# Kernel optimization log

Measured on AMD Instinct MI355X. Metric: run time of the kernel, lower is better.

The kernel has to match this reference:

```python
import jax, jax.numpy as jnp
import numpy as np

HEADS = 4
DIM_QK = 128
DIM_V = 128
FMAP = 32  # H = W = 32, L = 1024
DIM = 512
B = 16


def rel_to_abs(x):
    # x: [B, Nh, L, 2L-1] -> [B, Nh, L, L]
    b, nh, L, _ = x.shape
    x = jnp.pad(x, ((0, 0), (0, 0), (0, 0), (0, 1)))          # [B, Nh, L, 2L]
    flat = x.reshape(b, nh, L * 2 * L)
    flat = jnp.pad(flat, ((0, 0), (0, 0), (0, L - 1)))
    final = flat.reshape(b, nh, L + 1, 2 * L - 1)
    return final[:, :, :L, L - 1:]


def relative_logits_1d(q, rel_k):
    # q: [B, Nh, H, W, d], rel_k: [2W-1, d] -> [B, Nh, H, H, W, W]
    b, nh, h, w, _ = q.shape
    rl = jnp.einsum('bnhwd,md->bnhwm', q, rel_k)
    rl = rl.reshape(b, nh * h, w, 2 * w - 1)
    rl = rel_to_abs(rl)                                        # [B, Nh*H, W, W]
    rl = rl.reshape(b, nh, h, w, w)
    rl = jnp.broadcast_to(rl[:, :, :, None], (b, nh, h, h, w, w))
    return rl


def rel_pos_logits(q, rel_height, rel_width):
    # q: [B, Nh, L, d] with L = FMAP*FMAP -> [B, Nh, L, L]
    b, nh, L, d = q.shape
    h = w = FMAP
    q5 = q.reshape(b, nh, h, w, d)
    # width logits: 'b n x i y j -> b n (x y) (i j)'
    rw = relative_logits_1d(q5, rel_width)
    rw = rw.transpose(0, 1, 2, 4, 3, 5).reshape(b, nh, h * w, h * w)
    # height logits: transpose spatial, then 'b n x i y j -> b n (y x) (j i)'
    rh = relative_logits_1d(q5.transpose(0, 1, 3, 2, 4), rel_height)
    rh = rh.transpose(0, 1, 4, 2, 5, 3).reshape(b, nh, h * w, h * w)
    return rw + rh


def setup_inputs() -> dict:
    key = jax.random.key(0)
    k1, k2, k3, k4, k5 = jax.random.split(key, 5)
    scale = DIM_QK ** -0.5
    return {
        'featuremap': jax.random.normal(k1, (B, DIM, FMAP, FMAP), jnp.float32),
        'w_qk': jax.random.normal(k2, (2 * HEADS * DIM_QK, DIM), jnp.float32) * (DIM ** -0.5),
        'w_v': jax.random.normal(k3, (HEADS * DIM_V, DIM), jnp.float32) * (DIM ** -0.5),
        'rel_height': jax.random.normal(k4, (2 * FMAP - 1, DIM_QK), jnp.float32) * scale,
        'rel_width': jax.random.normal(k5, (2 * FMAP - 1, DIM_QK), jnp.float32) * scale,
    }


def reference(featuremap, w_qk, w_v, rel_height, rel_width):
    b, c, h, w = featuremap.shape
    L = h * w
    # 1x1 convs (no bias) == channel matmuls
    qk = jnp.einsum('bchw,oc->bohw', featuremap, w_qk)
    q, k = jnp.split(qk, 2, axis=1)
    v = jnp.einsum('bchw,oc->bohw', featuremap, w_v)

    def to_heads(x, d):
        # 'B (h d) H W -> B h (H W) d'
        return x.reshape(b, HEADS, d, L).transpose(0, 1, 3, 2)

    q = to_heads(q, DIM_QK) * (DIM_QK ** -0.5)
    k = to_heads(k, DIM_QK)
    v = to_heads(v, DIM_V)

    logits = jnp.einsum('bhxd,bhyd->bhxy', q, k)
    logits = logits + rel_pos_logits(q, rel_height, rel_width)
    weights = jax.nn.softmax(logits, axis=-1)
    attn = jnp.einsum('bhxy,bhyd->bhxd', weights, v)
    # 'B h (H W) d -> B (h d) H W'
    out = attn.transpose(0, 1, 3, 2).reshape(b, HEADS * DIM_V, h, w)
    return out
```

## Files before the change

### kernel.cpp

```cpp
#include <hip/hip_runtime.h>
#include <hip/hip_bf16.h>
#include <math.h>

typedef __bf16 bf16x8 __attribute__((ext_vector_type(8)));
typedef float f32x4 __attribute__((ext_vector_type(4)));

#define QSCALE_L2E (0.08838834764831845f * 1.4426950408889634f)

static __device__ __forceinline__ unsigned short bits_bf16(float v) {
  __hip_bfloat16 h = __float2bfloat16(v);
  return *reinterpret_cast<unsigned short*>(&h);
}

static __device__ __forceinline__ void gload16(const void* g, void* l) {
  __builtin_amdgcn_global_load_lds(
      (const __attribute__((address_space(1))) void*)g,
      (__attribute__((address_space(3))) void*)l, 16, 0, 0);
}

__global__ __launch_bounds__(256) void k_convw(const float* __restrict__ wqk,
                                               const float* __restrict__ wv,
                                               const float* __restrict__ relw,
                                               const float* __restrict__ relh,
                                               __hip_bfloat16* __restrict__ wall,
                                               __hip_bfloat16* __restrict__ relsb) {
  int i = blockIdx.x * 256 + threadIdx.x;
  if (i < 1536 * 512) {
    float v = (i < 1024 * 512) ? wqk[i] : wv[i - 1024 * 512];
    wall[i] = __float2bfloat16(v);
  } else {
    int j = i - 1536 * 512;
    int t = j >> 13, m = (j >> 7) & 63, d = j & 127;
    float v = (m < 63) ? (t ? relh[m * 128 + d] : relw[m * 128 + d]) : 0.f;
    relsb[j] = __float2bfloat16(v);
  }
}

__global__ __launch_bounds__(256) void k_tfm(const float* __restrict__ fm,
                                             __hip_bfloat16* __restrict__ fmt) {
  __shared__ float t[64][65];
  int lt = blockIdx.x, ct = blockIdx.y, b = blockIdx.z;
  int tid = threadIdx.x;
  const float* src = fm + ((size_t)b * 512 + ct * 64) * 1024 + lt * 64;
#pragma unroll
  for (int i = 0; i < 16; ++i) {
    int idx = i * 256 + tid;
    int r = idx >> 6, cl = idx & 63;
    t[r][cl] = src[(size_t)r * 1024 + cl];
  }
  __syncthreads();
  __hip_bfloat16* dst = fmt + ((size_t)b * 1024 + lt * 64) * 512 + ct * 64;
#pragma unroll
  for (int i = 0; i < 16; ++i) {
    int idx = i * 256 + tid;
    int r = idx >> 6, cc = idx & 63;
    dst[(size_t)r * 512 + cc] = __float2bfloat16(t[cc][r]);
  }
}

__global__ __launch_bounds__(256) void k_gemm(const __hip_bfloat16* __restrict__ fmt,
                                              const __hip_bfloat16* __restrict__ wall,
                                              __hip_bfloat16* __restrict__ Qb,
                                              __hip_bfloat16* __restrict__ Kb,
                                              __hip_bfloat16* __restrict__ Vt) {
  __shared__ char smem[32768];
  char* As = smem;
  char* Bs = smem + 16384;
  int bm = blockIdx.x, bn = blockIdx.y, b = blockIdx.z;
  int tid = threadIdx.x;
  int lane = tid & 63, wave = tid >> 6;
  int wr = wave >> 1, wc = wave & 1;
  int g = lane >> 4, ln = lane & 15;
  const char* Ag = (const char*)(fmt + ((size_t)b * 1024 + bm * 128) * 512);
  const char* Bg = (const char*)(wall + (size_t)bn * 128 * 512);

  int j3 = lane >> 3, j7 = lane & 7;
  int segsrc = ((j7 ^ j3) << 4);

  f32x4 acc[4][4] = {};
  for (int kb = 0; kb < 8; ++kb) {
#pragma unroll
    for (int i = 0; i < 4; ++i) {
      int R = (wave * 4 + i) * 8;
      size_t go = (size_t)(R + j3) * 1024 + (size_t)kb * 128 + segsrc;
      gload16(Ag + go, As + R * 128);
      gload16(Bg + go, Bs + R * 128);
    }
    __syncthreads();
#pragma unroll
    for (int ks = 0; ks < 2; ++ks) {
      int kcol = ks * 64 + (g << 4);
      bf16x8 af[4], bfr[4];
#pragma unroll
      for (int m = 0; m < 4; ++m) {
        int row = wr * 64 + m * 16 + ln;
        af[m] = *(const bf16x8*)(As + row * 128 + (kcol ^ ((ln & 7) << 4)));
      }
#pragma unroll
      for (int n = 0; n < 4; ++n) {
        int row = wc * 64 + n * 16 + ln;
        bfr[n] = *(const bf16x8*)(Bs + row * 128 + (kcol ^ ((ln & 7) << 4)));
      }
#pragma unroll
      for (int m = 0; m < 4; ++m)
#pragma unroll
        for (int n = 0; n < 4; ++n)
          acc[m][n] = __builtin_amdgcn_mfma_f32_16x16x32_bf16(af[m], bfr[n], acc[m][n], 0, 0, 0);
    }
    __syncthreads();
  }

  int otype = bn >> 2;
  int head = bn & 3;
  if (otype != 2) {
    float sc = (otype == 0) ? QSCALE_L2E : 1.0f;
#pragma unroll
    for (int m = 0; m < 4; ++m)
#pragma unroll
      for (int n = 0; n < 4; ++n) {
        int d = wc * 64 + n * 16 + ln;
#pragma unroll
        for (int r = 0; r < 4; ++r) {
          int l = wr * 64 + m * 16 + g * 4 + r;
          *(__hip_bfloat16*)(smem + l * 256 + ((d * 2) ^ ((l & 7) << 4))) =
              __float2bfloat16(acc[m][n][r] * sc);
        }
      }
    __syncthreads();
    __hip_bfloat16* dstb =
        (otype == 0 ? Qb : Kb) + (((size_t)(b * 4 + head) * 1024) + bm * 128) * 128;
#pragma unroll
    for (int i = 0; i < 8; ++i) {
      int idx = i * 256 + tid;
      int row = idx >> 4, c16 = idx & 15;
      uint4 v = *(const uint4*)(smem + row * 256 + ((c16 * 16) ^ ((row & 7) << 4)));
      *(uint4*)(dstb + (size_t)row * 128 + c16 * 8) = v;
    }
  } else {
#pragma unroll
    for (int m = 0; m < 4; ++m)
#pragma unroll
      for (int n = 0; n < 4; ++n) {
        int d = wc * 64 + n * 16 + ln;
        int lbase = wr * 64 + m * 16 + g * 4;
        ushort4 pk;
        pk.x = bits_bf16(acc[m][n][0]);
        pk.y = bits_bf16(acc[m][n][1]);
        pk.z = bits_bf16(acc[m][n][2]);
        pk.w = bits_bf16(acc[m][n][3]);
        *(ushort4*)(smem + d * 256 + ((lbase * 2) ^ ((d & 7) << 4))) = pk;
      }
    __syncthreads();
    __hip_bfloat16* dstb = Vt + ((size_t)(b * 4 + head) * 128) * 1024 + bm * 128;
#pragma unroll
    for (int i = 0; i < 8; ++i) {
      int idx = i * 256 + tid;
      int row = idx >> 4, c16 = idx & 15;
      uint4 v = *(const uint4*)(smem + row * 256 + ((c16 * 16) ^ ((row & 7) << 4)));
      *(uint4*)(dstb + (size_t)row * 1024 + c16 * 8) = v;
    }
  }
}

__global__ __launch_bounds__(256) void k_bias(const __hip_bfloat16* __restrict__ Qb,
                                              const __hip_bfloat16* __restrict__ relsb,
                                              float* __restrict__ QRW,
                                              float* __restrict__ QRH) {
  __shared__ char sh[32768];
  int bx = blockIdx.x, bh = blockIdx.y;
  int tid = threadIdx.x, lane = tid & 63, wave = tid >> 6;
  int g = lane >> 4, ln = lane & 15;
#pragma unroll
  for (int i = 0; i < 8; ++i) {
    int chunk = i * 256 + tid;
    int row = chunk >> 4, c16 = chunk & 15;
    *(uint4*)(sh + row * 256 + ((c16 * 16) ^ ((row & 7) << 4))) =
        *(const uint4*)(relsb + (size_t)row * 128 + c16 * 8);
  }
  __syncthreads();
  size_t bhL = (size_t)bh * 1024;
  int l0 = bx * 128 + wave * 32;
  const __hip_bfloat16* Qg = Qb + (bhL + l0) * 128;
  bf16x8 a[2][4];
#pragma unroll
  for (int lf = 0; lf < 2; ++lf)
#pragma unroll
    for (int ks = 0; ks < 4; ++ks)
      a[lf][ks] = *(const bf16x8*)(Qg + (size_t)(lf * 16 + ln) * 128 + ks * 32 + g * 8);
#pragma unroll
  for (int t = 0; t < 2; ++t) {
    float* dst = (t == 0 ? QRW : QRH) + (bhL + l0) * 64;
#pragma unroll
    for (int n = 0; n < 4; ++n) {
      f32x4 acc2[2] = {};
#pragma unroll
      for (int ks = 0; ks < 4; ++ks) {
        int mrow = n * 16 + ln;
        bf16x8 bf = *(const bf16x8*)(sh + t * 16384 + mrow * 256 +
                                     ((ks * 64 + g * 16) ^ ((mrow & 7) << 4)));
#pragma unroll
        for (int lf = 0; lf < 2; ++lf)
          acc2[lf] = __builtin_amdgcn_mfma_f32_16x16x32_bf16(a[lf][ks], bf, acc2[lf], 0, 0, 0);
      }
#pragma unroll
      for (int lf = 0; lf < 2; ++lf)
#pragma unroll
        for (int r = 0; r < 4; ++r)
          dst[(size_t)(lf * 16 + g * 4 + r) * 64 + n * 16 + ln] = acc2[lf][r];
    }
  }
}

__global__ __launch_bounds__(256) void k_attn(const __hip_bfloat16* __restrict__ Qb,
                                              const __hip_bfloat16* __restrict__ Kb,
                                              const __hip_bfloat16* __restrict__ Vt,
                                              const float* __restrict__ QRW,
                                              const float* __restrict__ QRH,
                                              float* __restrict__ out) {
  extern __shared__ char smem[];
  float* qrw_s = (float*)smem;
  float* qrh_s = (float*)(smem + 17408);
  char* kv = smem + 34816;
  char* vtl = smem + 51200;
  char* pt = smem + 67584;

  int qt = blockIdx.x, bh = blockIdx.y;
  int b = bh >> 2, h = bh & 3;
  int tid = threadIdx.x, lane = tid & 63, wave = tid >> 6;
  int g = lane >> 4, ln = lane & 15;
  int q0 = qt * 64;
  size_t bhL = (size_t)bh * 1024;

  const char* Qg = (const char*)(Qb + (bhL + q0) * 128);
#pragma unroll
  for (int i = 0; i < 4; ++i) {
    int R = (wave * 4 + i) * 4;
    int seg = ((lane & 15) ^ (((i & 1) * 4) + (lane >> 4))) << 4;
    gload16(Qg + (size_t)(R + (lane >> 4)) * 256 + seg, kv + R * 256);
  }
#pragma unroll
  for (int i = 0; i < 4; ++i) {
    int chunk = i * 256 + tid;
    int row = chunk >> 4, c16 = chunk & 15;
    *(uint4*)(qrw_s + row * 68 + c16 * 4) =
        *(const uint4*)(QRW + (bhL + q0 + row) * 64 + c16 * 4);
    *(uint4*)(qrh_s + row * 68 + c16 * 4) =
        *(const uint4*)(QRH + (bhL + q0 + row) * 64 + c16 * 4);
  }
  __syncthreads();

  bf16x8 qa[4];
  int qloc = wave * 16 + ln;
#pragma unroll
  for (int ks = 0; ks < 4; ++ks)
    qa[ks] = *(const bf16x8*)(kv + qloc * 256 + ((ks * 64 + (g << 4)) ^ ((qloc & 7) << 4)));

  int qg2 = q0 + qloc;
  int cx = qg2 & 31, rx = qg2 >> 5;
  float wb[2][4];
#pragma unroll
  for (int half = 0; half < 2; ++half)
#pragma unroll
    for (int r = 0; r < 4; ++r)
      wb[half][r] = qrw_s[qloc * 68 + (half * 16 + g * 4 + r - cx + 31)];
  const float* hptr = qrh_s + qloc * 68 + (31 - rx);

  f32x4 acc_o[8] = {};
  float mrow = -1e30f, lrow = 0.f;
  char* pw = pt + wave * 2048;
  const char* Kg0 = (const char*)(Kb + bhL * 128);
  const char* Vg0 = (const char*)(Vt + (size_t)bh * 128 * 1024);
  int j3 = lane >> 3, j7 = lane & 7;
  int segv = ((j7 ^ j3) << 4);

  for (int kt = 0; kt < 16; ++kt) {
    __syncthreads();
    const char* Kg = Kg0 + (size_t)kt * 64 * 256;
#pragma unroll
    for (int i = 0; i < 4; ++i) {
      int R = (wave * 4 + i) * 4;
      int seg = ((lane & 15) ^ (((i & 1) * 4) + (lane >> 4))) << 4;
      gload16(Kg + (size_t)(R + (lane >> 4)) * 256 + seg, kv + R * 256);
    }
    const char* Vg = Vg0 + (size_t)kt * 128;
#pragma unroll
    for (int i = 0; i < 4; ++i) {
      int R = (wave * 4 + i) * 8;
      gload16(Vg + (size_t)(R + j3) * 2048 + segv, vtl + R * 128);
    }
    __syncthreads();

    f32x4 s[4] = {};
#pragma unroll
    for (int ks = 0; ks < 4; ++ks) {
      int kcol = ks * 64 + (g << 4);
#pragma unroll
      for (int n = 0; n < 4; ++n) {
        int krow = n * 16 + ln;
        bf16x8 kf = *(const bf16x8*)(kv + krow * 256 + (kcol ^ ((krow & 7) << 4)));
        s[n] = __builtin_amdgcn_mfma_f32_16x16x32_bf16(kf, qa[ks], s[n], 0, 0, 0);
      }
    }
    float hb0 = hptr[kt * 2], hb1 = hptr[kt * 2 + 1];
#pragma unroll
    for (int n = 0; n < 4; ++n) {
      float hb = (n >> 1) ? hb1 : hb0;
#pragma unroll
      for (int r = 0; r < 4; ++r) s[n][r] += wb[n & 1][r] + hb;
    }
    float mt = s[0][0];
#pragma unroll
    for (int n = 0; n < 4; ++n)
#pragma unroll
      for (int r = 0; r < 4; ++r) mt = fmaxf(mt, s[n][r]);
    mt = fmaxf(mt, __shfl_xor(mt, 16, 64));
    mt = fmaxf(mt, __shfl_xor(mt, 32, 64));
    float mn = fmaxf(mrow, mt);
    float alpha = exp2f(mrow - mn);
    mrow = mn;
    float rs = 0.f;
#pragma unroll
    for (int n = 0; n < 4; ++n)
#pragma unroll
      for (int r = 0; r < 4; ++r) {
        s[n][r] = exp2f(s[n][r] - mrow);
        rs += s[n][r];
      }
    rs += __shfl_xor(rs, 16, 64);
    rs += __shfl_xor(rs, 32, 64);
    lrow = lrow * alpha + rs;
#pragma unroll
    for (int mf = 0; mf < 8; ++mf) acc_o[mf] *= alpha;
#pragma unroll
    for (int n = 0; n < 4; ++n) {
      ushort4 pk;
      pk.x = bits_bf16(s[n][0]);
      pk.y = bits_bf16(s[n][1]);
      pk.z = bits_bf16(s[n][2]);
      pk.w = bits_bf16(s[n][3]);
      *(ushort4*)(pw + ln * 128 + ((n * 32 + g * 8) ^ ((ln & 7) << 4))) = pk;
    }
#pragma unroll
    for (int ks2 = 0; ks2 < 2; ++ks2) {
      int kcb = ks2 * 64 + (g << 4);
      bf16x8 pb = *(const bf16x8*)(pw + ln * 128 + (kcb ^ ((ln & 7) << 4)));
#pragma unroll
      for (int mf = 0; mf < 8; ++mf) {
        int vrow = mf * 16 + ln;
        bf16x8 av = *(const bf16x8*)(vtl + vrow * 128 + (kcb ^ ((vrow & 7) << 4)));
        acc_o[mf] = __builtin_amdgcn_mfma_f32_16x16x32_bf16(av, pb, acc_o[mf], 0, 0, 0);
      }
    }
  }
  float linv = 1.0f / lrow;
  int qg3 = q0 + wave * 16 + ln;
#pragma unroll
  for (int mf = 0; mf < 8; ++mf) {
    int dbase = mf * 16 + g * 4;
#pragma unroll
    for (int r = 0; r < 4; ++r) {
      out[((size_t)(b * 512 + h * 128 + dbase + r)) * 1024 + qg3] = acc_o[mf][r] * linv;
    }
  }
}

extern "C" void kernel_launch(void* const* d_in, const int* in_sizes, int n_in,
                              void* d_out, int out_size, void* d_ws, size_t ws_size,
                              hipStream_t stream) {
  const float* fm = (const float*)d_in[0];
  const float* wqk = (const float*)d_in[1];
  const float* wv = (const float*)d_in[2];
  const float* relh = (const float*)d_in[3];
  const float* relw = (const float*)d_in[4];
  float* out = (float*)d_out;
  char* w = (char*)d_ws;

  __hip_bfloat16* fmt = (__hip_bfloat16*)w;
  __hip_bfloat16* wall = (__hip_bfloat16*)(w + 16777216);
  __hip_bfloat16* Qb = (__hip_bfloat16*)(w + 18350080);
  __hip_bfloat16* Kb = (__hip_bfloat16*)(w + 35127296);
  __hip_bfloat16* Vt = (__hip_bfloat16*)(w + 51904512);
  float* QRW = (float*)(w + 68681728);
  float* QRH = (float*)(w + 85458944);
  __hip_bfloat16* relsb = (__hip_bfloat16*)(w + 102236160);

  k_convw<<<3136, 256, 0, stream>>>(wqk, wv, relw, relh, wall, relsb);
  k_tfm<<<dim3(16, 8, 16), 256, 0, stream>>>(fm, fmt);
  k_gemm<<<dim3(8, 12, 16), 256, 0, stream>>>(fmt, wall, Qb, Kb, Vt);
  k_bias<<<dim3(8, 64), 256, 0, stream>>>(Qb, relsb, QRW, QRH);
  k_attn<<<dim3(16, 64), 256, 75776, stream>>>(Qb, Kb, Vt, QRW, QRH, out);
}
```

Measured before the change: 144.2 us.

## Process 128 queries per attention block, two row tiles per wave

```diff
diff --git a/kernel.cpp b/kernel.cpp
--- a/kernel.cpp
+++ b/kernel.cpp
@@ -211,63 +211,59 @@
   }
 }
 
-__global__ __launch_bounds__(256) void k_attn(const __hip_bfloat16* __restrict__ Qb,
-                                              const __hip_bfloat16* __restrict__ Kb,
-                                              const __hip_bfloat16* __restrict__ Vt,
-                                              const float* __restrict__ QRW,
-                                              const float* __restrict__ QRH,
-                                              float* __restrict__ out) {
+__global__ __launch_bounds__(256, 2) void k_attn(const __hip_bfloat16* __restrict__ Qb,
+                                                 const __hip_bfloat16* __restrict__ Kb,
+                                                 const __hip_bfloat16* __restrict__ Vt,
+                                                 const float* __restrict__ QRW,
+                                                 const float* __restrict__ QRH,
+                                                 float* __restrict__ out) {
   extern __shared__ char smem[];
-  float* qrw_s = (float*)smem;
-  float* qrh_s = (float*)(smem + 17408);
-  char* kv = smem + 34816;
-  char* vtl = smem + 51200;
-  char* pt = smem + 67584;
+  float* hb_s = (float*)smem;
+  char* kv = smem + 20480;
+  char* vtl = smem + 36864;
+  char* pt = smem + 53248;
 
   int qt = blockIdx.x, bh = blockIdx.y;
   int b = bh >> 2, h = bh & 3;
   int tid = threadIdx.x, lane = tid & 63, wave = tid >> 6;
   int g = lane >> 4, ln = lane & 15;
-  int q0 = qt * 64;
+  int q0 = qt * 128;
   size_t bhL = (size_t)bh * 1024;
 
-  const char* Qg = (const char*)(Qb + (bhL + q0) * 128);
-#pragma unroll
-  for (int i = 0; i < 4; ++i) {
-    int R = (wave * 4 + i) * 4;
-    int seg = ((lane & 15) ^ (((i & 1) * 4) + (lane >> 4))) << 4;
-    gload16(Qg + (size_t)(R + (lane >> 4)) * 256 + seg, kv + R * 256);
-  }
-#pragma unroll
-  for (int i = 0; i < 4; ++i) {
-    int chunk = i * 256 + tid;
-    int row = chunk >> 4, c16 = chunk & 15;
-    *(uint4*)(qrw_s + row * 68 + c16 * 4) =
-        *(const uint4*)(QRW + (bhL + q0 + row) * 64 + c16 * 4);
-    *(uint4*)(qrh_s + row * 68 + c16 * 4) =
-        *(const uint4*)(QRH + (bhL + q0 + row) * 64 + c16 * 4);
-  }
-  __syncthreads();
-
-  bf16x8 qa[4];
-  int qloc = wave * 16 + ln;
-#pragma unroll
-  for (int ks = 0; ks < 4; ++ks)
-    qa[ks] = *(const bf16x8*)(kv + qloc * 256 + ((ks * 64 + (g << 4)) ^ ((qloc & 7) << 4)));
-
-  int qg2 = q0 + qloc;
-  int cx = qg2 & 31, rx = qg2 >> 5;
-  float wb[2][4];
-#pragma unroll
-  for (int half = 0; half < 2; ++half)
-#pragma unroll
-    for (int r = 0; r < 4; ++r)
-      wb[half][r] = qrw_s[qloc * 68 + (half * 16 + g * 4 + r - cx + 31)];
-  const float* hptr = qrh_s + qloc * 68 + (31 - rx);
-
-  f32x4 acc_o[8] = {};
-  float mrow = -1e30f, lrow = 0.f;
-  char* pw = pt + wave * 2048;
+#pragma unroll
+  for (int i = 0; i < 5; ++i) {
+    int c = i * 256 + tid;
+    if (c < 1152) {
+      int row = c / 9, j = c % 9;
+      int s0 = (31 - ((q0 + row) >> 5)) & ~3;
+      *(uint4*)(hb_s + row * 40 + j * 4) =
+          *(const uint4*)(QRH + (bhL + q0 + row) * 64 + s0 + j * 4);
+    }
+  }
+
+  bf16x8 qa[2][4];
+  float wb[2][2][4];
+  int qloc[2], hbase[2];
+#pragma unroll
+  for (int u = 0; u < 2; ++u) {
+    qloc[u] = wave * 32 + u * 16 + ln;
+    int qg = q0 + qloc[u];
+    int cx = qg & 31, rx = qg >> 5;
+    hbase[u] = (31 - rx) & 3;
+    const __hip_bfloat16* qrow = Qb + (bhL + qg) * 128;
+#pragma unroll
+    for (int ks = 0; ks < 4; ++ks)
+      qa[u][ks] = *(const bf16x8*)(qrow + ks * 32 + g * 8);
+    const float* wrow = QRW + (bhL + qg) * 64 + (31 - cx) + g * 4;
+#pragma unroll
+    for (int half = 0; half < 2; ++half)
+#pragma unroll
+      for (int r = 0; r < 4; ++r) wb[u][half][r] = wrow[half * 16 + r];
+  }
+
+  f32x4 acc[2][8] = {};
+  float mrow[2] = {-1e30f, -1e30f}, lrow[2] = {0.f, 0.f};
+  char* pw = pt + wave * 4096;
   const char* Kg0 = (const char*)(Kb + bhL * 128);
   const char* Vg0 = (const char*)(Vt + (size_t)bh * 128 * 1024);
   int j3 = lane >> 3, j7 = lane & 7;
@@ -290,7 +286,7 @@
     }
     __syncthreads();
 
-    f32x4 s[4] = {};
+    f32x4 s[2][4] = {};
 #pragma unroll
     for (int ks = 0; ks < 4; ++ks) {
       int kcol = ks * 64 + (g << 4);
@@ -298,68 +294,78 @@
       for (int n = 0; n < 4; ++n) {
         int krow = n * 16 + ln;
         bf16x8 kf = *(const bf16x8*)(kv + krow * 256 + (kcol ^ ((krow & 7) << 4)));
-        s[n] = __builtin_amdgcn_mfma_f32_16x16x32_bf16(kf, qa[ks], s[n], 0, 0, 0);
-      }
-    }
-    float hb0 = hptr[kt * 2], hb1 = hptr[kt * 2 + 1];
-#pragma unroll
-    for (int n = 0; n < 4; ++n) {
-      float hb = (n >> 1) ? hb1 : hb0;
-#pragma unroll
-      for (int r = 0; r < 4; ++r) s[n][r] += wb[n & 1][r] + hb;
-    }
-    float mt = s[0][0];
-#pragma unroll
-    for (int n = 0; n < 4; ++n)
-#pragma unroll
-      for (int r = 0; r < 4; ++r) mt = fmaxf(mt, s[n][r]);
-    mt = fmaxf(mt, __shfl_xor(mt, 16, 64));
-    mt = fmaxf(mt, __shfl_xor(mt, 32, 64));
-    float mn = fmaxf(mrow, mt);
-    float alpha = exp2f(mrow - mn);
-    mrow = mn;
-    float rs = 0.f;
-#pragma unroll
-    for (int n = 0; n < 4; ++n)
-#pragma unroll
-      for (int r = 0; r < 4; ++r) {
-        s[n][r] = exp2f(s[n][r] - mrow);
-        rs += s[n][r];
-      }
-    rs += __shfl_xor(rs, 16, 64);
-    rs += __shfl_xor(rs, 32, 64);
-    lrow = lrow * alpha + rs;
-#pragma unroll
-    for (int mf = 0; mf < 8; ++mf) acc_o[mf] *= alpha;
-#pragma unroll
-    for (int n = 0; n < 4; ++n) {
-      ushort4 pk;
-      pk.x = bits_bf16(s[n][0]);
-      pk.y = bits_bf16(s[n][1]);
-      pk.z = bits_bf16(s[n][2]);
-      pk.w = bits_bf16(s[n][3]);
-      *(ushort4*)(pw + ln * 128 + ((n * 32 + g * 8) ^ ((ln & 7) << 4))) = pk;
+        s[0][n] = __builtin_amdgcn_mfma_f32_16x16x32_bf16(kf, qa[0][ks], s[0][n], 0, 0, 0);
+        s[1][n] = __builtin_amdgcn_mfma_f32_16x16x32_bf16(kf, qa[1][ks], s[1][n], 0, 0, 0);
+      }
+    }
+#pragma unroll
+    for (int u = 0; u < 2; ++u) {
+      float hb0 = hb_s[qloc[u] * 40 + hbase[u] + kt * 2];
+      float hb1 = hb_s[qloc[u] * 40 + hbase[u] + kt * 2 + 1];
+#pragma unroll
+      for (int n = 0; n < 4; ++n) {
+        float hb = (n >> 1) ? hb1 : hb0;
+#pragma unroll
+        for (int r = 0; r < 4; ++r) s[u][n][r] += wb[u][n & 1][r] + hb;
+      }
+      float mt = s[u][0][0];
+#pragma unroll
+      for (int n = 0; n < 4; ++n)
+#pragma unroll
+        for (int r = 0; r < 4; ++r) mt = fmaxf(mt, s[u][n][r]);
+      mt = fmaxf(mt, __shfl_xor(mt, 16, 64));
+      mt = fmaxf(mt, __shfl_xor(mt, 32, 64));
+      float mn = fmaxf(mrow[u], mt);
+      float alpha = exp2f(mrow[u] - mn);
+      mrow[u] = mn;
+      float rs = 0.f;
+#pragma unroll
+      for (int n = 0; n < 4; ++n)
+#pragma unroll
+        for (int r = 0; r < 4; ++r) {
+          s[u][n][r] = exp2f(s[u][n][r] - mn);
+          rs += s[u][n][r];
+        }
+      rs += __shfl_xor(rs, 16, 64);
+      rs += __shfl_xor(rs, 32, 64);
+      lrow[u] = lrow[u] * alpha + rs;
+#pragma unroll
+      for (int mf = 0; mf < 8; ++mf) acc[u][mf] *= alpha;
+#pragma unroll
+      for (int n = 0; n < 4; ++n) {
+        ushort4 pk;
+        pk.x = bits_bf16(s[u][n][0]);
+        pk.y = bits_bf16(s[u][n][1]);
+        pk.z = bits_bf16(s[u][n][2]);
+        pk.w = bits_bf16(s[u][n][3]);
+        *(ushort4*)(pw + (u * 16 + ln) * 128 + ((n * 32 + g * 8) ^ ((ln & 7) << 4))) = pk;
+      }
     }
 #pragma unroll
     for (int ks2 = 0; ks2 < 2; ++ks2) {
       int kcb = ks2 * 64 + (g << 4);
-      bf16x8 pb = *(const bf16x8*)(pw + ln * 128 + (kcb ^ ((ln & 7) << 4)));
+      bf16x8 pb0 = *(const bf16x8*)(pw + ln * 128 + (kcb ^ ((ln & 7) << 4)));
+      bf16x8 pb1 = *(const bf16x8*)(pw + (16 + ln) * 128 + (kcb ^ ((ln & 7) << 4)));
 #pragma unroll
       for (int mf = 0; mf < 8; ++mf) {
         int vrow = mf * 16 + ln;
         bf16x8 av = *(const bf16x8*)(vtl + vrow * 128 + (kcb ^ ((vrow & 7) << 4)));
-        acc_o[mf] = __builtin_amdgcn_mfma_f32_16x16x32_bf16(av, pb, acc_o[mf], 0, 0, 0);
-      }
-    }
-  }
-  float linv = 1.0f / lrow;
-  int qg3 = q0 + wave * 16 + ln;
-#pragma unroll
-  for (int mf = 0; mf < 8; ++mf) {
-    int dbase = mf * 16 + g * 4;
-#pragma unroll
-    for (int r = 0; r < 4; ++r) {
-      out[((size_t)(b * 512 + h * 128 + dbase + r)) * 1024 + qg3] = acc_o[mf][r] * linv;
+        acc[0][mf] = __builtin_amdgcn_mfma_f32_16x16x32_bf16(av, pb0, acc[0][mf], 0, 0, 0);
+        acc[1][mf] = __builtin_amdgcn_mfma_f32_16x16x32_bf16(av, pb1, acc[1][mf], 0, 0, 0);
+      }
+    }
+  }
+#pragma unroll
+  for (int u = 0; u < 2; ++u) {
+    float linv = 1.0f / lrow[u];
+    int qg3 = q0 + wave * 32 + u * 16 + ln;
+#pragma unroll
+    for (int mf = 0; mf < 8; ++mf) {
+      int dbase = mf * 16 + g * 4;
+#pragma unroll
+      for (int r = 0; r < 4; ++r) {
+        out[((size_t)(b * 512 + h * 128 + dbase + r)) * 1024 + qg3] = acc[u][mf][r] * linv;
+      }
     }
   }
 }
@@ -388,5 +394,5 @@
   k_tfm<<<dim3(16, 8, 16), 256, 0, stream>>>(fm, fmt);
   k_gemm<<<dim3(8, 12, 16), 256, 0, stream>>>(fmt, wall, Qb, Kb, Vt);
   k_bias<<<dim3(8, 64), 256, 0, stream>>>(Qb, relsb, QRW, QRH);
-  k_attn<<<dim3(16, 64), 256, 75776, stream>>>(Qb, Kb, Vt, QRW, QRH, out);
-}
+  k_attn<<<dim3(8, 64), 256, 69632, stream>>>(Qb, Kb, Vt, QRW, QRH, out);
+}
```

New measurement: 132.1 us. 8.4% less time.

## Double-buffer K/V tiles in attention kernel with 512-thread blocks and lazy rescale

Applied to the files above, without the earlier changes.

```diff
diff --git a/kernel.cpp b/kernel.cpp
--- a/kernel.cpp
+++ b/kernel.cpp
@@ -211,97 +211,96 @@
   }
 }
 
-__global__ __launch_bounds__(256) void k_attn(const __hip_bfloat16* __restrict__ Qb,
-                                              const __hip_bfloat16* __restrict__ Kb,
-                                              const __hip_bfloat16* __restrict__ Vt,
-                                              const float* __restrict__ QRW,
-                                              const float* __restrict__ QRH,
-                                              float* __restrict__ out) {
+__global__ __launch_bounds__(512, 4) void k_attn(const __hip_bfloat16* __restrict__ Qb,
+                                                 const __hip_bfloat16* __restrict__ Kb,
+                                                 const __hip_bfloat16* __restrict__ Vt,
+                                                 const float* __restrict__ QRW,
+                                                 const float* __restrict__ QRH,
+                                                 float* __restrict__ out) {
   extern __shared__ char smem[];
-  float* qrw_s = (float*)smem;
-  float* qrh_s = (float*)(smem + 17408);
-  char* kv = smem + 34816;
-  char* vtl = smem + 51200;
-  char* pt = smem + 67584;
-
-  int qt = blockIdx.x, bh = blockIdx.y;
+  char* kb0 = smem;
+  char* kb1 = smem + 16384;
+  char* vb0 = smem + 32768;
+  char* vb1 = smem + 49152;
+  char* pt = smem + 65536;
+
+  int bh = blockIdx.x, qt = blockIdx.y;
   int b = bh >> 2, h = bh & 3;
   int tid = threadIdx.x, lane = tid & 63, wave = tid >> 6;
   int g = lane >> 4, ln = lane & 15;
-  int q0 = qt * 64;
+  int q0 = qt * 128;
   size_t bhL = (size_t)bh * 1024;
 
-  const char* Qg = (const char*)(Qb + (bhL + q0) * 128);
-#pragma unroll
-  for (int i = 0; i < 4; ++i) {
-    int R = (wave * 4 + i) * 4;
-    int seg = ((lane & 15) ^ (((i & 1) * 4) + (lane >> 4))) << 4;
-    gload16(Qg + (size_t)(R + (lane >> 4)) * 256 + seg, kv + R * 256);
-  }
-#pragma unroll
-  for (int i = 0; i < 4; ++i) {
-    int chunk = i * 256 + tid;
-    int row = chunk >> 4, c16 = chunk & 15;
-    *(uint4*)(qrw_s + row * 68 + c16 * 4) =
-        *(const uint4*)(QRW + (bhL + q0 + row) * 64 + c16 * 4);
-    *(uint4*)(qrh_s + row * 68 + c16 * 4) =
-        *(const uint4*)(QRH + (bhL + q0 + row) * 64 + c16 * 4);
-  }
-  __syncthreads();
-
+  int qloc = wave * 16 + ln;
+  int qg = q0 + qloc;
+  int cx = qg & 31, rx = qg >> 5;
   bf16x8 qa[4];
-  int qloc = wave * 16 + ln;
-#pragma unroll
-  for (int ks = 0; ks < 4; ++ks)
-    qa[ks] = *(const bf16x8*)(kv + qloc * 256 + ((ks * 64 + (g << 4)) ^ ((qloc & 7) << 4)));
-
-  int qg2 = q0 + qloc;
-  int cx = qg2 & 31, rx = qg2 >> 5;
+  const __hip_bfloat16* qrow = Qb + (bhL + qg) * 128;
+#pragma unroll
+  for (int ks = 0; ks < 4; ++ks) qa[ks] = *(const bf16x8*)(qrow + ks * 32 + g * 8);
   float wb[2][4];
+  const float* wrow = QRW + (bhL + qg) * 64 + (31 - cx) + g * 4;
 #pragma unroll
   for (int half = 0; half < 2; ++half)
 #pragma unroll
-    for (int r = 0; r < 4; ++r)
-      wb[half][r] = qrw_s[qloc * 68 + (half * 16 + g * 4 + r - cx + 31)];
-  const float* hptr = qrh_s + qloc * 68 + (31 - rx);
-
-  f32x4 acc_o[8] = {};
-  float mrow = -1e30f, lrow = 0.f;
-  char* pw = pt + wave * 2048;
+    for (int r = 0; r < 4; ++r) wb[half][r] = wrow[half * 16 + r];
+  const float* hptr = QRH + (bhL + qg) * 64 + (31 - rx);
+
   const char* Kg0 = (const char*)(Kb + bhL * 128);
   const char* Vg0 = (const char*)(Vt + (size_t)bh * 128 * 1024);
   int j3 = lane >> 3, j7 = lane & 7;
   int segv = ((j7 ^ j3) << 4);
 
+  auto STAGE_K = [&](char* kvb, int kt2) {
+    const char* Kg = Kg0 + (size_t)kt2 * 64 * 256;
+#pragma unroll
+    for (int i = 0; i < 2; ++i) {
+      int R = (wave * 2 + i) * 4;
+      int seg = ((lane & 15) ^ ((i & 1) * 4 + (lane >> 4))) << 4;
+      gload16(Kg + (size_t)(R + (lane >> 4)) * 256 + seg, kvb + R * 256);
+    }
+  };
+  auto STAGE_V = [&](char* vtb, int kt2) {
+    const char* Vg = Vg0 + (size_t)kt2 * 128;
+#pragma unroll
+    for (int i = 0; i < 2; ++i) {
+      int R = (wave * 2 + i) * 8;
+      gload16(Vg + (size_t)(R + j3) * 2048 + segv, vtb + R * 128);
+    }
+  };
+
+  f32x4 acc[8] = {};
+  float mrow = -1e30f, lrow = 0.f;
+  char* pw = pt + wave * 2048;
+
+  STAGE_K(kb0, 0);
+  STAGE_V(vb0, 0);
+  __syncthreads();
+
+  char *kc = kb0, *kn = kb1, *vc = vb0, *vn = vb1;
+
+#pragma unroll 1
   for (int kt = 0; kt < 16; ++kt) {
-    __syncthreads();
-    const char* Kg = Kg0 + (size_t)kt * 64 * 256;
-#pragma unroll
-    for (int i = 0; i < 4; ++i) {
-      int R = (wave * 4 + i) * 4;
-      int seg = ((lane & 15) ^ (((i & 1) * 4) + (lane >> 4))) << 4;
-      gload16(Kg + (size_t)(R + (lane >> 4)) * 256 + seg, kv + R * 256);
-    }
-    const char* Vg = Vg0 + (size_t)kt * 128;
-#pragma unroll
-    for (int i = 0; i < 4; ++i) {
-      int R = (wave * 4 + i) * 8;
-      gload16(Vg + (size_t)(R + j3) * 2048 + segv, vtl + R * 128);
-    }
-    __syncthreads();
+    if (kt < 15) {
+      STAGE_K(kn, kt + 1);
+      STAGE_V(vn, kt + 1);
+    }
+    float hb0 = hptr[kt * 2], hb1 = hptr[kt * 2 + 1];
 
     f32x4 s[4] = {};
+    __builtin_amdgcn_s_setprio(1);
 #pragma unroll
     for (int ks = 0; ks < 4; ++ks) {
       int kcol = ks * 64 + (g << 4);
 #pragma unroll
       for (int n = 0; n < 4; ++n) {
         int krow = n * 16 + ln;
-        bf16x8 kf = *(const bf16x8*)(kv + krow * 256 + (kcol ^ ((krow & 7) << 4)));
+        bf16x8 kf = *(const bf16x8*)(kc + krow * 256 + (kcol ^ ((krow & 7) << 4)));
         s[n] = __builtin_amdgcn_mfma_f32_16x16x32_bf16(kf, qa[ks], s[n], 0, 0, 0);
       }
     }
-    float hb0 = hptr[kt * 2], hb1 = hptr[kt * 2 + 1];
+    __builtin_amdgcn_s_setprio(0);
+
 #pragma unroll
     for (int n = 0; n < 4; ++n) {
       float hb = (n >> 1) ? hb1 : hb0;
@@ -315,9 +314,14 @@
       for (int r = 0; r < 4; ++r) mt = fmaxf(mt, s[n][r]);
     mt = fmaxf(mt, __shfl_xor(mt, 16, 64));
     mt = fmaxf(mt, __shfl_xor(mt, 32, 64));
-    float mn = fmaxf(mrow, mt);
-    float alpha = exp2f(mrow - mn);
-    mrow = mn;
+    if (__any(mt > mrow + 8.f)) {
+      float mn = fmaxf(mrow, mt);
+      float alpha = exp2f(mrow - mn);
+      mrow = mn;
+      lrow *= alpha;
+#pragma unroll
+      for (int mf = 0; mf < 8; ++mf) acc[mf] *= alpha;
+    }
     float rs = 0.f;
 #pragma unroll
     for (int n = 0; n < 4; ++n)
@@ -328,9 +332,8 @@
       }
     rs += __shfl_xor(rs, 16, 64);
     rs += __shfl_xor(rs, 32, 64);
-    lrow = lrow * alpha + rs;
-#pragma unroll
-    for (int mf = 0; mf < 8; ++mf) acc_o[mf] *= alpha;
+    lrow += rs;
+
 #pragma unroll
     for (int n = 0; n < 4; ++n) {
       ushort4 pk;
@@ -340,6 +343,7 @@
       pk.w = bits_bf16(s[n][3]);
       *(ushort4*)(pw + ln * 128 + ((n * 32 + g * 8) ^ ((ln & 7) << 4))) = pk;
     }
+    __builtin_amdgcn_s_setprio(1);
 #pragma unroll
     for (int ks2 = 0; ks2 < 2; ++ks2) {
       int kcb = ks2 * 64 + (g << 4);
@@ -347,19 +351,24 @@
 #pragma unroll
       for (int mf = 0; mf < 8; ++mf) {
         int vrow = mf * 16 + ln;
-        bf16x8 av = *(const bf16x8*)(vtl + vrow * 128 + (kcb ^ ((vrow & 7) << 4)));
-        acc_o[mf] = __builtin_amdgcn_mfma_f32_16x16x32_bf16(av, pb, acc_o[mf], 0, 0, 0);
-      }
-    }
-  }
+        bf16x8 av = *(const bf16x8*)(vc + vrow * 128 + (kcb ^ ((vrow & 7) << 4)));
+        acc[mf] = __builtin_amdgcn_mfma_f32_16x16x32_bf16(av, pb, acc[mf], 0, 0, 0);
+      }
+    }
+    __builtin_amdgcn_s_setprio(0);
+
+    __syncthreads();
+    char* t = kc; kc = kn; kn = t;
+    char* t2 = vc; vc = vn; vn = t2;
+  }
+
   float linv = 1.0f / lrow;
-  int qg3 = q0 + wave * 16 + ln;
 #pragma unroll
   for (int mf = 0; mf < 8; ++mf) {
     int dbase = mf * 16 + g * 4;
 #pragma unroll
     for (int r = 0; r < 4; ++r) {
-      out[((size_t)(b * 512 + h * 128 + dbase + r)) * 1024 + qg3] = acc_o[mf][r] * linv;
+      out[((size_t)(b * 512 + h * 128 + dbase + r)) * 1024 + qg] = acc[mf][r] * linv;
     }
   }
 }
@@ -384,9 +393,12 @@
   float* QRH = (float*)(w + 85458944);
   __hip_bfloat16* relsb = (__hip_bfloat16*)(w + 102236160);
 
+  hipFuncSetAttribute((const void*)k_attn,
+                      hipFuncAttributeMaxDynamicSharedMemorySize, 81920);
+
   k_convw<<<3136, 256, 0, stream>>>(wqk, wv, relw, relh, wall, relsb);
   k_tfm<<<dim3(16, 8, 16), 256, 0, stream>>>(fm, fmt);
   k_gemm<<<dim3(8, 12, 16), 256, 0, stream>>>(fmt, wall, Qb, Kb, Vt);
   k_bias<<<dim3(8, 64), 256, 0, stream>>>(Qb, relsb, QRW, QRH);
-  k_attn<<<dim3(16, 64), 256, 75776, stream>>>(Qb, Kb, Vt, QRW, QRH, out);
-}
+  k_attn<<<dim3(64, 8), 512, 81920, stream>>>(Qb, Kb, Vt, QRW, QRH, out);
+}
```

Measured after the change: 122.0 us (median of 2 runs). 1.18x faster.
